# Performance work log

Measured on AMD Instinct MI355X. Metric: run time of the kernel, lower is better.

The kernel has to match this reference:

```python
import jax, jax.numpy as jnp
import numpy as np

DIM = 256
NUM_HEADS = 4
HEAD_DIM = DIM // NUM_HEADS  # 64
SCALE = HEAD_DIM ** -0.5


def _dwconv(x, w, b):
    # x: [B,H,W,C], w: [3,3,1,C] depthwise, stride 2, padding 1
    c = x.shape[-1]
    y = jax.lax.conv_general_dilated(
        x, w, window_strides=(2, 2), padding=((1, 1), (1, 1)),
        dimension_numbers=('NHWC', 'HWIO', 'NHWC'), feature_group_count=c)
    return y + b


def setup_inputs() -> dict:
    key = jax.random.key(0)
    ks = jax.random.split(key, 12)
    s = 0.02
    return {
        'x': jax.random.normal(ks[0], (8, 64, 64, DIM), jnp.float32),
        'q_w': jax.random.normal(ks[1], (DIM, DIM), jnp.float32) * s,
        'q_b': jnp.zeros((DIM,), jnp.float32),
        'k_w': jax.random.normal(ks[2], (DIM, HEAD_DIM), jnp.float32) * s,
        'k_b': jnp.zeros((HEAD_DIM,), jnp.float32),
        'v_w': jax.random.normal(ks[3], (DIM, HEAD_DIM), jnp.float32) * s,
        'v_b': jnp.zeros((HEAD_DIM,), jnp.float32),
        'kconv_w': jax.random.normal(ks[4], (3, 3, 1, HEAD_DIM), jnp.float32) * s,
        'kconv_b': jnp.zeros((HEAD_DIM,), jnp.float32),
        'vconv_w': jax.random.normal(ks[5], (3, 3, 1, HEAD_DIM), jnp.float32) * s,
        'vconv_b': jnp.zeros((HEAD_DIM,), jnp.float32),
        'out_w': jax.random.normal(ks[6], (DIM, DIM), jnp.float32) * s,
        'out_b': jnp.zeros((DIM,), jnp.float32),
    }


def reference(x, q_w, q_b, k_w, k_b, v_w, v_b,
              kconv_w, kconv_b, vconv_w, vconv_b, out_w, out_b):
    B, H, W, _ = x.shape
    S = H * W
    q = x @ q_w + q_b                      # [B,H,W,DIM]
    k = x @ k_w + k_b                      # [B,H,W,HEAD_DIM]
    v = x @ v_w + v_b
    k = _dwconv(k, kconv_w, kconv_b)       # [B,H/2,W/2,HEAD_DIM]
    v = _dwconv(v, vconv_w, vconv_b)
    Kv = (H // 2) * (W // 2)
    q = q.reshape(B, S, NUM_HEADS, HEAD_DIM)
    k = k.reshape(B, Kv, HEAD_DIM)
    v = v.reshape(B, Kv, HEAD_DIM)
    # MQA: single shared K/V head
    attn = jnp.einsum('bqhd,bkd->bhqk', q, k) * SCALE
    attn = jax.nn.softmax(attn, axis=-1)
    out = jnp.einsum('bhqk,bkd->bqhd', attn, v)   # [B,S,nh,hd]
    out = out.reshape(B, S, DIM) @ out_w + out_b
    return out.reshape(B, H, W, DIM)
```

## Files before the change

### kernel.cpp

```cpp
#include <hip/hip_runtime.h>
#include <hip/hip_bf16.h>

typedef __bf16 v8bf __attribute__((ext_vector_type(8)));
typedef float f32x4 __attribute__((ext_vector_type(4)));
typedef float f32x16 __attribute__((ext_vector_type(16)));
typedef int v2i __attribute__((ext_vector_type(2)));
typedef int v4i __attribute__((ext_vector_type(4)));

#define MFMA16(a, b, c) __builtin_amdgcn_mfma_f32_16x16x32_bf16(a, b, c, 0, 0, 0)
#define MFMA32(a, b, c) __builtin_amdgcn_mfma_f32_32x32x16_bf16(a, b, c, 0, 0, 0)
#define GLOAD16(gp, lp)                                                        \
  __builtin_amdgcn_global_load_lds(                                            \
      (const __attribute__((address_space(1))) void*)(gp),                     \
      (__attribute__((address_space(3))) void*)(lp), 16, 0, 0)

#define QSCALE 0.18033688011112042f

__global__ __launch_bounds__(256) void k_cvt_w(const float* __restrict__ qw,
                                               const float* __restrict__ kw,
                                               const float* __restrict__ vw,
                                               const float* __restrict__ ow,
                                               __bf16* __restrict__ wfrag,
                                               __bf16* __restrict__ owfrag) {
  int t = blockIdx.x * 256 + threadIdx.x;
  if (t < 98304) {
    int e = t & 7, idx = t >> 3;
    int l = idx & 63; idx >>= 6;
    int n = idx & 3; idx >>= 2;
    int kk = idx & 7, nb = idx >> 3;
    int nn = nb * 64 + n * 16 + (l & 15);
    int k = kk * 32 + 8 * (l >> 4) + e;
    float v;
    if (nn < 256) v = qw[k * 256 + nn] * QSCALE;
    else if (nn < 320) v = kw[k * 64 + (nn - 256)];
    else v = vw[k * 64 + (nn - 320)];
    wfrag[t] = (__bf16)v;
  } else {
    int u = t - 98304;
    int e = u & 7, idx = u >> 3;
    int l = idx & 63; idx >>= 6;
    int n = idx & 3; idx >>= 2;
    int kk = idx & 7, nb = idx >> 3;
    int nn = nb * 64 + n * 16 + (l & 15);
    int k = kk * 32 + 8 * (l >> 4) + e;
    owfrag[u] = (__bf16)ow[k * 256 + nn];
  }
}

__global__ __launch_bounds__(256) void k_qkv(const float* __restrict__ x,
                                             const __bf16* __restrict__ wfrag,
                                             const float* __restrict__ qb,
                                             const float* __restrict__ kb,
                                             const float* __restrict__ vb,
                                             __bf16* __restrict__ qo,
                                             __bf16* __restrict__ klin,
                                             __bf16* __restrict__ vlin) {
  int bx = blockIdx.x;
  int L = (bx & 7) * 128 + (bx >> 3);
  int mb = L >> 1, nh = L & 1;
  int wave = threadIdx.x >> 6, lane = threadIdx.x & 63;
  int g = lane >> 4, c = lane & 15;
  int r0 = mb * 64 + wave * 16;
  const v8bf* wf = (const v8bf*)wfrag;

  v8bf a[8];
#pragma unroll
  for (int kk = 0; kk < 8; ++kk) {
    const float* ap = x + (size_t)(r0 + c) * 256 + kk * 32 + 8 * g;
    float4 f0 = *(const float4*)ap;
    float4 f1 = *(const float4*)(ap + 4);
    v8bf t;
    t[0] = (__bf16)f0.x; t[1] = (__bf16)f0.y; t[2] = (__bf16)f0.z; t[3] = (__bf16)f0.w;
    t[4] = (__bf16)f1.x; t[5] = (__bf16)f1.y; t[6] = (__bf16)f1.z; t[7] = (__bf16)f1.w;
    a[kk] = t;
  }
#pragma unroll
  for (int ni = 0; ni < 3; ++ni) {
    int nb = nh * 3 + ni;
    int n0 = nb * 64;
    f32x4 acc[4];
#pragma unroll
    for (int n = 0; n < 4; ++n) acc[n] = f32x4{0.f, 0.f, 0.f, 0.f};
#pragma unroll
    for (int kk = 0; kk < 8; ++kk) {
      v8bf bf[4];
#pragma unroll
      for (int n = 0; n < 4; ++n)
        bf[n] = wf[(((nb * 8 + kk) * 4 + n) << 6) | lane];
#pragma unroll
      for (int n = 0; n < 4; ++n) acc[n] = MFMA16(a[kk], bf[n], acc[n]);
    }
#pragma unroll
    for (int n = 0; n < 4; ++n) {
      int col = n0 + n * 16 + c;
      float bias;
      if (col < 256) bias = qb[col] * QSCALE;
      else if (col < 320) bias = kb[col - 256];
      else bias = vb[col - 320];
#pragma unroll
      for (int j = 0; j < 4; ++j) {
        int row = r0 + 4 * g + j;
        float v = acc[n][j] + bias;
        if (col < 256) qo[(size_t)row * 256 + col] = (__bf16)v;
        else if (col < 320) klin[(size_t)row * 64 + (col - 256)] = (__bf16)v;
        else vlin[(size_t)row * 64 + (col - 320)] = (__bf16)v;
      }
    }
  }
}

__global__ __launch_bounds__(256) void k_conv(const __bf16* __restrict__ klin,
                                              const __bf16* __restrict__ vlin,
                                              const float* __restrict__ kw,
                                              const float* __restrict__ kbias,
                                              const float* __restrict__ vw,
                                              const float* __restrict__ vbias,
                                              __bf16* __restrict__ kc,
                                              __bf16* __restrict__ vcT) {
  __shared__ __bf16 VT[32][66];
  int bx = blockIdx.x;
  int b = bx >> 5, pt = bx & 31;
  int t = threadIdx.x;
  int ch = t & 63, pg = t >> 6;
  float kwv[9], vwv[9];
#pragma unroll
  for (int i = 0; i < 9; ++i) { kwv[i] = kw[i * 64 + ch]; vwv[i] = vw[i * 64 + ch]; }
  float kb0 = kbias[ch], vb0 = vbias[ch];
  const __bf16* kin = klin + (size_t)b * 262144;
  const __bf16* vin = vlin + (size_t)b * 262144;
#pragma unroll
  for (int i = 0; i < 8; ++i) {
    int pl = pg * 8 + i;
    int p = pt * 32 + pl;
    int oy = p >> 5, ox = p & 31;
    float ak = kb0, av = vb0;
#pragma unroll
    for (int dy = 0; dy < 3; ++dy) {
      int iy = 2 * oy - 1 + dy;
      if (iy < 0 || iy > 63) continue;
#pragma unroll
      for (int dx = 0; dx < 3; ++dx) {
        int ix = 2 * ox - 1 + dx;
        if (ix < 0 || ix > 63) continue;
        size_t src = ((size_t)iy * 64 + ix) * 64 + ch;
        ak += (float)kin[src] * kwv[dy * 3 + dx];
        av += (float)vin[src] * vwv[dy * 3 + dx];
      }
    }
    kc[((size_t)b * 1024 + p) * 64 + ch] = (__bf16)ak;
    VT[pl][ch] = (__bf16)av;
  }
  __syncthreads();
  int row = t >> 2, c0 = (t & 3) * 8;
  __bf16 tmp[8];
#pragma unroll
  for (int i = 0; i < 8; ++i) tmp[i] = VT[c0 + i][row];
  *(v4i*)(vcT + (size_t)b * 65536 + row * 1024 + pt * 32 + c0) = *(v4i*)tmp;
}

__global__ __launch_bounds__(256) void k_attn(const __bf16* __restrict__ q,
                                              const __bf16* __restrict__ kc,
                                              const __bf16* __restrict__ vcT,
                                              __bf16* __restrict__ pv) {
  __shared__ __bf16 KV[8192];
  int bx = blockIdx.x;
  int L = (bx & 7) * 128 + (bx >> 3);
  int b = L >> 7, hq = L & 127;
  int h = hq >> 5, qg = hq & 31;
  int wave = threadIdx.x >> 6, lane = threadIdx.x & 63;
  int c = lane & 31, hi = lane >> 5;
  int t = threadIdx.x;
  int qtile = qg * 4 + wave;
  size_t rowBase = (size_t)b * 4096 + qtile * 32;

  int kj = t >> 5, kr = (t & 31) ^ kj;
  const __bf16* kg = kc + (size_t)b * 65536 + kr * 64 + kj * 8;
  int dt_ = t >> 7, ks_ = (t >> 6) & 1, vh_ = (t >> 5) & 1;
  int cc = (t & 31) ^ (ks_ * 2 + vh_);
  const __bf16* vg = vcT + (size_t)b * 65536 + (size_t)(dt_ * 32 + cc) * 1024 +
                     ks_ * 16 + vh_ * 8;
  __bf16* kl = &KV[t * 8];
  __bf16* vl = &KV[2048 + t * 8];

  int Koff[4], Voff[2][2];
#pragma unroll
  for (int kk = 0; kk < 4; ++kk) {
    int j = kk * 2 + hi;
    Koff[kk] = (j * 32 + (c ^ j)) * 8;
  }
#pragma unroll
  for (int ks = 0; ks < 2; ++ks)
#pragma unroll
    for (int dt = 0; dt < 2; ++dt) {
      int j = ks * 2 + hi;
      Voff[ks][dt] = (256 + dt * 128 + ks * 64 + hi * 32 + (c ^ j)) * 8;
    }

  const __bf16* qbase = q + (rowBase + c) * 256 + h * 64 + hi * 8;
  v8bf Qf[4];
#pragma unroll
  for (int kk = 0; kk < 4; ++kk) Qf[kk] = *(const v8bf*)(qbase + kk * 16);

  f32x16 O0 = {}, O1 = {};
  const f32x16 Z16 = {};
  float ls0 = 0.f, ls1 = 0.f, ls2 = 0.f, ls3 = 0.f;

  GLOAD16(kg, kl);
  GLOAD16(vg, vl);
  __syncthreads();

  int buf = 0;
  for (int it = 0; it < 32; ++it) {
    const __bf16* base = &KV[buf * 4096];
    v8bf Kf[4], Vf[2][2];
#pragma unroll
    for (int kk = 0; kk < 4; ++kk) Kf[kk] = *(const v8bf*)(base + Koff[kk]);
#pragma unroll
    for (int ks = 0; ks < 2; ++ks)
#pragma unroll
      for (int dt = 0; dt < 2; ++dt)
        Vf[ks][dt] = *(const v8bf*)(base + Voff[ks][dt]);

    if (it < 31) {
      int nb = buf ^ 1;
      GLOAD16(kg + (it + 1) * 2048, kl + nb * 4096);
      GLOAD16(vg + (it + 1) * 32, vl + nb * 4096);
    }

    f32x16 S = MFMA32(Kf[0], Qf[0], Z16);
    S = MFMA32(Kf[1], Qf[1], S);
    S = MFMA32(Kf[2], Qf[2], S);
    S = MFMA32(Kf[3], Qf[3], S);

    float p[16];
#pragma unroll
    for (int r = 0; r < 16; ++r) p[r] = __builtin_amdgcn_exp2f(S[r]);
    ls0 += (p[0] + p[1]) + (p[2] + p[3]);
    ls1 += (p[4] + p[5]) + (p[6] + p[7]);
    ls2 += (p[8] + p[9]) + (p[10] + p[11]);
    ls3 += (p[12] + p[13]) + (p[14] + p[15]);

    int w[8];
#pragma unroll
    for (int q2 = 0; q2 < 8; ++q2) {
      int r;
      asm("v_cvt_pk_bf16_f32 %0, %1, %2" : "=v"(r) : "v"(p[2 * q2]), "v"(p[2 * q2 + 1]));
      w[q2] = r;
    }
    v2i s1 = __builtin_amdgcn_permlane32_swap(w[2], w[0], false, false);
    v2i s2 = __builtin_amdgcn_permlane32_swap(w[3], w[1], false, false);
    v2i s3 = __builtin_amdgcn_permlane32_swap(w[6], w[4], false, false);
    v2i s4 = __builtin_amdgcn_permlane32_swap(w[7], w[5], false, false);
    v4i pa0i, pa1i;
    pa0i[0] = s1[1]; pa0i[1] = s2[1]; pa0i[2] = s1[0]; pa0i[3] = s2[0];
    pa1i[0] = s3[1]; pa1i[1] = s4[1]; pa1i[2] = s3[0]; pa1i[3] = s4[0];
    v8bf pa0 = *(v8bf*)&pa0i, pa1 = *(v8bf*)&pa1i;

    O0 = MFMA32(pa0, Vf[0][0], O0);
    O1 = MFMA32(pa0, Vf[0][1], O1);
    O0 = MFMA32(pa1, Vf[1][0], O0);
    O1 = MFMA32(pa1, Vf[1][1], O1);

    __syncthreads();
    buf ^= 1;
  }

  float lsum = (ls0 + ls1) + (ls2 + ls3);
  float tot = lsum + __shfl_xor(lsum, 32);
  float linv = 1.0f / tot;
  __bf16* op = pv + rowBase * 256 + h * 64;
#pragma unroll
  for (int r = 0; r < 16; ++r) {
    int qr = (r & 3) + 8 * (r >> 2) + 4 * hi;
    float li = __shfl(linv, qr);
    op[(size_t)qr * 256 + c] = (__bf16)(O0[r] * li);
    op[(size_t)qr * 256 + 32 + c] = (__bf16)(O1[r] * li);
  }
}

__global__ __launch_bounds__(256) void k_out(const __bf16* __restrict__ pvb,
                                             const __bf16* __restrict__ owfrag,
                                             const float* __restrict__ ob,
                                             float* __restrict__ out) {
  int bx = blockIdx.x;
  int L = (bx & 7) * 128 + (bx >> 3);
  int mb = L >> 1, nh = L & 1;
  int wave = threadIdx.x >> 6, lane = threadIdx.x & 63;
  int g = lane >> 4, c = lane & 15;
  int r0 = mb * 64 + wave * 16;
  const v8bf* wf = (const v8bf*)owfrag;

  v8bf a[8];
#pragma unroll
  for (int kk = 0; kk < 8; ++kk)
    a[kk] = *(const v8bf*)(pvb + (size_t)(r0 + c) * 256 + kk * 32 + 8 * g);
#pragma unroll
  for (int ni = 0; ni < 2; ++ni) {
    int nb = nh * 2 + ni;
    int n0 = nb * 64;
    f32x4 acc[4];
#pragma unroll
    for (int n = 0; n < 4; ++n) acc[n] = f32x4{0.f, 0.f, 0.f, 0.f};
#pragma unroll
    for (int kk = 0; kk < 8; ++kk) {
      v8bf bf[4];
#pragma unroll
      for (int n = 0; n < 4; ++n)
        bf[n] = wf[(((nb * 8 + kk) * 4 + n) << 6) | lane];
#pragma unroll
      for (int n = 0; n < 4; ++n) acc[n] = MFMA16(a[kk], bf[n], acc[n]);
    }
#pragma unroll
    for (int n = 0; n < 4; ++n) {
      int col = n0 + n * 16 + c;
      float bias = ob[col];
#pragma unroll
      for (int j = 0; j < 4; ++j) {
        int row = r0 + 4 * g + j;
        out[(size_t)row * 256 + col] = acc[n][j] + bias;
      }
    }
  }
}

extern "C" void kernel_launch(void* const* d_in, const int* in_sizes, int n_in,
                              void* d_out, int out_size, void* d_ws, size_t ws_size,
                              hipStream_t stream) {
  const float* x   = (const float*)d_in[0];
  const float* qw  = (const float*)d_in[1];
  const float* qb  = (const float*)d_in[2];
  const float* kw  = (const float*)d_in[3];
  const float* kb  = (const float*)d_in[4];
  const float* vw  = (const float*)d_in[5];
  const float* vb  = (const float*)d_in[6];
  const float* kcw = (const float*)d_in[7];
  const float* kcb = (const float*)d_in[8];
  const float* vcw = (const float*)d_in[9];
  const float* vcb = (const float*)d_in[10];
  const float* ow  = (const float*)d_in[11];
  const float* ob  = (const float*)d_in[12];
  float* out = (float*)d_out;
  char* ws = (char*)d_ws;

  __bf16* pv     = (__bf16*)(ws + 0);
  __bf16* qbuf   = (__bf16*)(ws + 16777216);
  __bf16* klin   = (__bf16*)(ws + 33554432);
  __bf16* vlin   = (__bf16*)(ws + 37748736);
  __bf16* kc     = (__bf16*)(ws + 41943040);
  __bf16* vcT    = (__bf16*)(ws + 42991616);
  __bf16* wfrag  = (__bf16*)(ws + 44040192);
  __bf16* owfrag = (__bf16*)(ws + 44236800);

  k_cvt_w<<<640, 256, 0, stream>>>(qw, kw, vw, ow, wfrag, owfrag);
  k_qkv<<<1024, 256, 0, stream>>>(x, wfrag, qb, kb, vb, qbuf, klin, vlin);
  k_conv<<<256, 256, 0, stream>>>(klin, vlin, kcw, kcb, vcw, vcb, kc, vcT);
  k_attn<<<1024, 256, 0, stream>>>(qbuf, kc, vcT, pv);
  k_out<<<1024, 256, 0, stream>>>(pv, owfrag, ob, out);
}
```

Measured before the change: 106.5 us.

## Fuse output projection into attention kernel and merge QKV column halves per block

The attention kernel now assigns each block one 32-row query tile across all four heads, one head per wave. It stages the normalized head outputs in shared memory and performs the output projection plus bias directly, so the separate output-projection kernel and its bf16 intermediate buffer round trip are removed. The QKV kernel now has each block compute all six 64-column groups for its rows, halving the grid and avoiding a second fp32 read and conversion of x per row block. The cost is more serial work per block in both kernels and less parallelism in QKV.

```diff
diff --git a/kernel.cpp b/kernel.cpp
--- a/kernel.cpp
+++ b/kernel.cpp
@@ -56,8 +56,7 @@
                                              __bf16* __restrict__ klin,
                                              __bf16* __restrict__ vlin) {
   int bx = blockIdx.x;
-  int L = (bx & 7) * 128 + (bx >> 3);
-  int mb = L >> 1, nh = L & 1;
+  int mb = (bx & 7) * 64 + (bx >> 3);
   int wave = threadIdx.x >> 6, lane = threadIdx.x & 63;
   int g = lane >> 4, c = lane & 15;
   int r0 = mb * 64 + wave * 16;
@@ -75,8 +74,7 @@
     a[kk] = t;
   }
 #pragma unroll
-  for (int ni = 0; ni < 3; ++ni) {
-    int nb = nh * 3 + ni;
+  for (int nb = 0; nb < 6; ++nb) {
     int n0 = nb * 64;
     f32x4 acc[4];
 #pragma unroll
@@ -161,17 +159,17 @@
 __global__ __launch_bounds__(256) void k_attn(const __bf16* __restrict__ q,
                                               const __bf16* __restrict__ kc,
                                               const __bf16* __restrict__ vcT,
-                                              __bf16* __restrict__ pv) {
-  __shared__ __bf16 KV[8192];
+                                              const __bf16* __restrict__ owfrag,
+                                              const float* __restrict__ ob,
+                                              float* __restrict__ out) {
+  __shared__ __bf16 SMEM[8448];
   int bx = blockIdx.x;
   int L = (bx & 7) * 128 + (bx >> 3);
-  int b = L >> 7, hq = L & 127;
-  int h = hq >> 5, qg = hq & 31;
+  int b = L >> 7, qt = L & 127;
   int wave = threadIdx.x >> 6, lane = threadIdx.x & 63;
   int c = lane & 31, hi = lane >> 5;
   int t = threadIdx.x;
-  int qtile = qg * 4 + wave;
-  size_t rowBase = (size_t)b * 4096 + qtile * 32;
+  size_t rowBase = (size_t)b * 4096 + qt * 32;
 
   int kj = t >> 5, kr = (t & 31) ^ kj;
   const __bf16* kg = kc + (size_t)b * 65536 + kr * 64 + kj * 8;
@@ -179,8 +177,8 @@
   int cc = (t & 31) ^ (ks_ * 2 + vh_);
   const __bf16* vg = vcT + (size_t)b * 65536 + (size_t)(dt_ * 32 + cc) * 1024 +
                      ks_ * 16 + vh_ * 8;
-  __bf16* kl = &KV[t * 8];
-  __bf16* vl = &KV[2048 + t * 8];
+  __bf16* kl = &SMEM[t * 8];
+  __bf16* vl = &SMEM[2048 + t * 8];
 
   int Koff[4], Voff[2][2];
 #pragma unroll
@@ -196,7 +194,7 @@
       Voff[ks][dt] = (256 + dt * 128 + ks * 64 + hi * 32 + (c ^ j)) * 8;
     }
 
-  const __bf16* qbase = q + (rowBase + c) * 256 + h * 64 + hi * 8;
+  const __bf16* qbase = q + (rowBase + c) * 256 + wave * 64 + hi * 8;
   v8bf Qf[4];
 #pragma unroll
   for (int kk = 0; kk < 4; ++kk) Qf[kk] = *(const v8bf*)(qbase + kk * 16);
@@ -211,7 +209,7 @@
 
   int buf = 0;
   for (int it = 0; it < 32; ++it) {
-    const __bf16* base = &KV[buf * 4096];
+    const __bf16* base = &SMEM[buf * 4096];
     v8bf Kf[4], Vf[2][2];
 #pragma unroll
     for (int kk = 0; kk < 4; ++kk) Kf[kk] = *(const v8bf*)(base + Koff[kk]);
@@ -232,19 +230,19 @@
     S = MFMA32(Kf[2], Qf[2], S);
     S = MFMA32(Kf[3], Qf[3], S);
 
-    float p[16];
-#pragma unroll
-    for (int r = 0; r < 16; ++r) p[r] = __builtin_amdgcn_exp2f(S[r]);
-    ls0 += (p[0] + p[1]) + (p[2] + p[3]);
-    ls1 += (p[4] + p[5]) + (p[6] + p[7]);
-    ls2 += (p[8] + p[9]) + (p[10] + p[11]);
-    ls3 += (p[12] + p[13]) + (p[14] + p[15]);
+#pragma unroll
+    for (int r = 0; r < 16; ++r) S[r] = __builtin_amdgcn_exp2f(S[r]);
+    ls0 += (S[0] + S[1]) + (S[2] + S[3]);
+    ls1 += (S[4] + S[5]) + (S[6] + S[7]);
+    ls2 += (S[8] + S[9]) + (S[10] + S[11]);
+    ls3 += (S[12] + S[13]) + (S[14] + S[15]);
 
     int w[8];
 #pragma unroll
     for (int q2 = 0; q2 < 8; ++q2) {
       int r;
-      asm("v_cvt_pk_bf16_f32 %0, %1, %2" : "=v"(r) : "v"(p[2 * q2]), "v"(p[2 * q2 + 1]));
+      asm("v_cvt_pk_bf16_f32 %0, %1, %2"
+          : "=v"(r) : "v"(S[2 * q2]), "v"(S[2 * q2 + 1]));
       w[q2] = r;
     }
     v2i s1 = __builtin_amdgcn_permlane32_swap(w[2], w[0], false, false);
@@ -268,58 +266,49 @@
   float lsum = (ls0 + ls1) + (ls2 + ls3);
   float tot = lsum + __shfl_xor(lsum, 32);
   float linv = 1.0f / tot;
-  __bf16* op = pv + rowBase * 256 + h * 64;
+
+  __bf16(*Ot)[264] = (__bf16(*)[264])SMEM;
 #pragma unroll
   for (int r = 0; r < 16; ++r) {
     int qr = (r & 3) + 8 * (r >> 2) + 4 * hi;
     float li = __shfl(linv, qr);
-    op[(size_t)qr * 256 + c] = (__bf16)(O0[r] * li);
-    op[(size_t)qr * 256 + 32 + c] = (__bf16)(O1[r] * li);
-  }
-}
-
-__global__ __launch_bounds__(256) void k_out(const __bf16* __restrict__ pvb,
-                                             const __bf16* __restrict__ owfrag,
-                                             const float* __restrict__ ob,
-                                             float* __restrict__ out) {
-  int bx = blockIdx.x;
-  int L = (bx & 7) * 128 + (bx >> 3);
-  int mb = L >> 1, nh = L & 1;
-  int wave = threadIdx.x >> 6, lane = threadIdx.x & 63;
-  int g = lane >> 4, c = lane & 15;
-  int r0 = mb * 64 + wave * 16;
+    Ot[qr][wave * 64 + c] = (__bf16)(O0[r] * li);
+    Ot[qr][wave * 64 + 32 + c] = (__bf16)(O1[r] * li);
+  }
+  __syncthreads();
+
+  int g = lane >> 4, c16 = lane & 15;
   const v8bf* wf = (const v8bf*)owfrag;
-
-  v8bf a[8];
-#pragma unroll
-  for (int kk = 0; kk < 8; ++kk)
-    a[kk] = *(const v8bf*)(pvb + (size_t)(r0 + c) * 256 + kk * 32 + 8 * g);
-#pragma unroll
-  for (int ni = 0; ni < 2; ++ni) {
-    int nb = nh * 2 + ni;
-    int n0 = nb * 64;
-    f32x4 acc[4];
-#pragma unroll
-    for (int n = 0; n < 4; ++n) acc[n] = f32x4{0.f, 0.f, 0.f, 0.f};
-#pragma unroll
-    for (int kk = 0; kk < 8; ++kk) {
-      v8bf bf[4];
-#pragma unroll
-      for (int n = 0; n < 4; ++n)
-        bf[n] = wf[(((nb * 8 + kk) * 4 + n) << 6) | lane];
-#pragma unroll
-      for (int n = 0; n < 4; ++n) acc[n] = MFMA16(a[kk], bf[n], acc[n]);
-    }
+  f32x4 acc[2][4];
+#pragma unroll
+  for (int m = 0; m < 2; ++m)
+#pragma unroll
+    for (int n = 0; n < 4; ++n) acc[m][n] = f32x4{0.f, 0.f, 0.f, 0.f};
+#pragma unroll
+  for (int kk = 0; kk < 8; ++kk) {
+    v8bf a0 = *(const v8bf*)&Ot[c16][kk * 32 + 8 * g];
+    v8bf a1 = *(const v8bf*)&Ot[16 + c16][kk * 32 + 8 * g];
+    v8bf bf[4];
+#pragma unroll
+    for (int n = 0; n < 4; ++n)
+      bf[n] = wf[(((wave * 8 + kk) * 4 + n) << 6) | lane];
 #pragma unroll
     for (int n = 0; n < 4; ++n) {
-      int col = n0 + n * 16 + c;
-      float bias = ob[col];
+      acc[0][n] = MFMA16(a0, bf[n], acc[0][n]);
+      acc[1][n] = MFMA16(a1, bf[n], acc[1][n]);
+    }
+  }
+#pragma unroll
+  for (int n = 0; n < 4; ++n) {
+    int col = wave * 64 + n * 16 + c16;
+    float bias = ob[col];
+#pragma unroll
+    for (int m = 0; m < 2; ++m)
 #pragma unroll
       for (int j = 0; j < 4; ++j) {
-        int row = r0 + 4 * g + j;
-        out[(size_t)row * 256 + col] = acc[n][j] + bias;
+        int row = m * 16 + 4 * g + j;
+        out[(rowBase + row) * 256 + col] = acc[m][n][j] + bias;
       }
-    }
   }
 }
 
@@ -342,7 +331,6 @@
   float* out = (float*)d_out;
   char* ws = (char*)d_ws;
 
-  __bf16* pv     = (__bf16*)(ws + 0);
   __bf16* qbuf   = (__bf16*)(ws + 16777216);
   __bf16* klin   = (__bf16*)(ws + 33554432);
   __bf16* vlin   = (__bf16*)(ws + 37748736);
@@ -352,8 +340,7 @@
   __bf16* owfrag = (__bf16*)(ws + 44236800);
 
   k_cvt_w<<<640, 256, 0, stream>>>(qw, kw, vw, ow, wfrag, owfrag);
-  k_qkv<<<1024, 256, 0, stream>>>(x, wfrag, qb, kb, vb, qbuf, klin, vlin);
+  k_qkv<<<512, 256, 0, stream>>>(x, wfrag, qb, kb, vb, qbuf, klin, vlin);
   k_conv<<<256, 256, 0, stream>>>(klin, vlin, kcw, kcb, vcw, vcb, kc, vcT);
-  k_attn<<<1024, 256, 0, stream>>>(qbuf, kc, vcT, pv);
-  k_out<<<1024, 256, 0, stream>>>(pv, owfrag, ob, out);
-}
+  k_attn<<<1024, 256, 0, stream>>>(qbuf, kc, vcT, owfrag, ob, out);
+}
```

Result: no change. 107.1 us (+0.6%).
